# Kernel optimization log

Measured on AMD Instinct MI355X. Metric: run time of the kernel, lower is better.

Reference implementation:

```python
import jax, jax.numpy as jnp
import numpy as np

L, H, NH, NKV, HD, FF, E, K = 4, 1024, 16, 4, 64, 2048, 8, 2
B, S = 2, 2048
THETA, EPS = 10000.0, 1e-5


def setup_inputs() -> dict:
    key = jax.random.key(0)
    ks = jax.random.split(key, 12)
    sc = 0.02
    inp = {
        "hidden_states": jax.random.normal(ks[0], (B, S, H), jnp.float32),
        "ln1_w": jnp.ones((L, H), jnp.float32),
        "ln2_w": jnp.ones((L, H), jnp.float32),
        "wq": jax.random.normal(ks[1], (L, H, NH * HD), jnp.float32) * sc,
        "wk": jax.random.normal(ks[2], (L, H, NKV * HD), jnp.float32) * sc,
        "wv": jax.random.normal(ks[3], (L, H, NKV * HD), jnp.float32) * sc,
        "wo": jax.random.normal(ks[4], (L, NH * HD, H), jnp.float32) * sc,
        "wr": jax.random.normal(ks[5], (L, H, E), jnp.float32) * sc,
        "wg": jax.random.normal(ks[6], (L, E, H, FF), jnp.float32) * sc,
        "wu": jax.random.normal(ks[7], (L, E, H, FF), jnp.float32) * sc,
        "wd": jax.random.normal(ks[8], (L, E, FF, H), jnp.float32) * sc,
    }
    return inp


def _rms(x, w):
    return x * jax.lax.rsqrt(jnp.mean(x * x, axis=-1, keepdims=True) + EPS) * w


def _rope_cos_sin(seq_len, head_dim, theta):
    inv = 1.0 / (theta ** (jnp.arange(0, head_dim, 2, dtype=jnp.float32) / head_dim))
    f = jnp.arange(seq_len, dtype=jnp.float32)[:, None] * inv  # [S, HD/2]
    emb = jnp.concatenate([f, f], axis=-1)  # [S, HD]
    return jnp.cos(emb), jnp.sin(emb)


def _rot_half(x):
    h = x.shape[-1] // 2
    return jnp.concatenate([-x[..., h:], x[..., :h]], axis=-1)


def _attention(x, wq, wk, wv, wo, cos, sin, causal_bias):
    b, s, _ = x.shape
    q = (x @ wq).reshape(b, s, NH, HD).transpose(0, 2, 1, 3)   # [B,NH,S,HD]
    k = (x @ wk).reshape(b, s, NKV, HD).transpose(0, 2, 1, 3)  # [B,NKV,S,HD]
    v = (x @ wv).reshape(b, s, NKV, HD).transpose(0, 2, 1, 3)
    c = cos[None, None]
    sn = sin[None, None]
    q = q * c + _rot_half(q) * sn
    k = k * c + _rot_half(k) * sn
    rep = NH // NKV
    k = jnp.repeat(k, rep, axis=1)  # [B,NH,S,HD]
    v = jnp.repeat(v, rep, axis=1)
    scores = jnp.einsum("bhqd,bhkd->bhqk", q, k) / jnp.sqrt(jnp.asarray(HD, x.dtype))
    scores = scores + causal_bias  # [1,1,S,S] broadcast
    attn = jax.nn.softmax(scores, axis=-1)
    out = jnp.einsum("bhqk,bhkd->bhqd", attn, v)
    out = out.transpose(0, 2, 1, 3).reshape(b, s, NH * HD)
    return out @ wo


def _moe(x, wr, wg, wu, wd):
    logits = x @ wr                            # [B,S,E]
    probs = jax.nn.softmax(logits, axis=-1)
    topv, topi = jax.lax.top_k(probs, K)       # [B,S,K]
    topv = topv / jnp.sum(topv, axis=-1, keepdims=True)
    # dense per-expert combine weights [B,S,E]
    comb = jnp.sum(jax.nn.one_hot(topi, E, dtype=x.dtype) * topv[..., None], axis=-2)
    out = jnp.zeros_like(x)
    for e in range(E):  # fixed small expert count
        h = jax.nn.silu(x @ wg[e]) * (x @ wu[e])  # [B,S,FF]
        out = out + comb[..., e:e + 1] * (h @ wd[e])
    return out


def reference(hidden_states, ln1_w, ln2_w, wq, wk, wv, wo, wr, wg, wu, wd):
    s = hidden_states.shape[1]
    cos, sin = _rope_cos_sin(s, HD, THETA)
    causal_bias = jnp.where(
        jnp.tril(jnp.ones((s, s), bool))[None, None], 0.0, -1e9
    ).astype(hidden_states.dtype)
    x = hidden_states
    for l in range(L):
        res = x
        h = _rms(x, ln1_w[l])
        h = _attention(h, wq[l], wk[l], wv[l], wo[l], cos, sin, causal_bias)
        x = jnp.clip(res + h, -100.0, 100.0)
        res = x
        h = _rms(x, ln2_w[l])
        h = _moe(h, wr[l], wg[l], wu[l], wd[l])
        x = jnp.clip(res + h, -100.0, 100.0)
    return x
```

## Files before the change

kernel.cpp:

```cpp
#include <hip/hip_runtime.h>
#include <hip/hip_bf16.h>
#include <math.h>

typedef unsigned short u16;
typedef short short8 __attribute__((ext_vector_type(8)));
typedef short short4v __attribute__((ext_vector_type(4)));
typedef float f32x4 __attribute__((ext_vector_type(4)));

#define NLAYER 4
#define HDIM 1024
#define NHEAD 16
#define NKVH 4
#define FFDIM 2048
#define NEXP 8
#define SEQ 2048
#define NBATCH 2
#define NTOK (NBATCH*SEQ)
#define NPAIR (NTOK*2)
#define RMS_EPS 1e-5f

__device__ __forceinline__ u16 b16(float x) {
  union { __hip_bfloat16 h; u16 u; } c;
  c.h = __float2bfloat16(x);
  return c.u;
}
__device__ __forceinline__ float b2f(u16 b) {
  return __builtin_bit_cast(float, ((unsigned)b) << 16);
}
__device__ __forceinline__ void split2(float x, u16& o0, u16& o1) {
  o0 = b16(x); o1 = b16(x - b2f(o0));
}
__device__ __forceinline__ float clip100(float v) {
  return fminf(fmaxf(v, -100.f), 100.f);
}
__device__ __forceinline__ int swz8(int bid, int nwg) {
  return (bid & 7) * (nwg >> 3) + (bid >> 3);
}

__global__ __launch_bounds__(256)
void rmsnorm_kernel(const float* __restrict__ x, const float* __restrict__ w,
                    u16* __restrict__ oh, u16* __restrict__ ol) {
  int t = blockIdx.x, tid = threadIdx.x;
  const float* xr = x + (long)t * HDIM;
  float4 v = *(const float4*)(xr + tid * 4);
  float ss = v.x*v.x + v.y*v.y + v.z*v.z + v.w*v.w;
  #pragma unroll
  for (int m = 32; m; m >>= 1) ss += __shfl_xor(ss, m);
  __shared__ float sb[4];
  if ((tid & 63) == 0) sb[tid >> 6] = ss;
  __syncthreads();
  ss = sb[0] + sb[1] + sb[2] + sb[3];
  float sc = 1.0f / sqrtf(ss * (1.f/HDIM) + RMS_EPS);
  float4 wv = *(const float4*)(w + tid * 4);
  float ov[4] = {v.x*sc*wv.x, v.y*sc*wv.y, v.z*sc*wv.z, v.w*sc*wv.w};
  short4v hv, lv;
  #pragma unroll
  for (int j = 0; j < 4; j++) { u16 h, l; split2(ov[j], h, l); hv[j]=(short)h; lv[j]=(short)l; }
  *(short4v*)&oh[(long)t*HDIM + tid*4] = hv;
  *(short4v*)&ol[(long)t*HDIM + tid*4] = lv;
}

__global__ __launch_bounds__(256)
void rope_table_kernel(float* __restrict__ tab) {
  int idx = blockIdx.x * 256 + threadIdx.x;
  int i = idx & 31, pos = idx >> 5;
  double e = -(double)i * 0.28782313662425575;
  float inv = (float)exp(e);
  float f = (float)pos * inv;
  tab[idx] = cosf(f);
  tab[SEQ*32 + idx] = sinf(f);
}

#define GPAD 40

__device__ __forceinline__ void gemm_core128(
    const u16* __restrict__ Ah, const u16* __restrict__ Al, long arow,
    const float* __restrict__ Bp, int Nb, int bcol0, int K,
    u16 (&As)[2][128][GPAD], u16 (&Bs)[2][64][GPAD],
    int tid, int wr, int lr, int lg, f32x4 (&acc)[2][4])
{
  int a_r = tid >> 1, a_kq = (tid & 1) * 16;
  int b_col = tid & 63;
  int b_kh = (tid >> 6) * 8;
  short8 pA[4];
  float pB[8];
  short8 cBh, cBl;
  auto loadA = [&](int k0) {
    if (arow >= 0) {
      const u16* ah = Ah + arow * (long)K + k0 + a_kq;
      const u16* al = Al + arow * (long)K + k0 + a_kq;
      pA[0] = *(const short8*)ah;
      pA[1] = *(const short8*)(ah + 8);
      pA[2] = *(const short8*)al;
      pA[3] = *(const short8*)(al + 8);
    } else {
      short8 z = {0,0,0,0,0,0,0,0};
      #pragma unroll
      for (int q = 0; q < 4; q++) pA[q] = z;
    }
  };
  auto loadB = [&](int k0) {
    const float* bp = Bp + (long)(k0 + b_kh) * Nb + bcol0 + b_col;
    #pragma unroll
    for (int j = 0; j < 8; j++) pB[j] = bp[(long)j * Nb];
  };
  auto convB = [&]() {
    #pragma unroll
    for (int j = 0; j < 8; j++) {
      u16 h, l; split2(pB[j], h, l);
      cBh[j] = (short)h; cBl[j] = (short)l;
    }
  };
  loadA(0); loadB(0); convB();
  for (int k0 = 0; k0 < K; k0 += 32) {
    if (k0) __syncthreads();
    *(short8*)&As[0][a_r][a_kq]     = pA[0];
    *(short8*)&As[0][a_r][a_kq + 8] = pA[1];
    *(short8*)&As[1][a_r][a_kq]     = pA[2];
    *(short8*)&As[1][a_r][a_kq + 8] = pA[3];
    *(short8*)&Bs[0][b_col][b_kh] = cBh;
    *(short8*)&Bs[1][b_col][b_kh] = cBl;
    __syncthreads();
    int kn = k0 + 32;
    if (kn < K) { loadA(kn); loadB(kn); }
    short8 bf[2][4];
    #pragma unroll
    for (int t = 0; t < 2; t++)
      #pragma unroll
      for (int n = 0; n < 4; n++)
        bf[t][n] = *(const short8*)&Bs[t][n*16 + lr][lg*8];
    #pragma unroll
    for (int m = 0; m < 2; m++) {
      short8 afh = *(const short8*)&As[0][wr + m*16 + lr][lg*8];
      short8 afl = *(const short8*)&As[1][wr + m*16 + lr][lg*8];
      #pragma unroll
      for (int n = 0; n < 4; n++) {
        f32x4 a = acc[m][n];
        a = __builtin_amdgcn_mfma_f32_16x16x32_bf16(afh, bf[0][n], a, 0, 0, 0);
        a = __builtin_amdgcn_mfma_f32_16x16x32_bf16(afh, bf[1][n], a, 0, 0, 0);
        a = __builtin_amdgcn_mfma_f32_16x16x32_bf16(afl, bf[0][n], a, 0, 0, 0);
        acc[m][n] = a;
      }
    }
    if (kn < K) convB();
  }
}

__global__ __launch_bounds__(256)
void gemm_down(const u16* __restrict__ Ah, const u16* __restrict__ Al,
               const float* __restrict__ B, float* __restrict__ Cf,
               const int* __restrict__ offs, int N, int K, long bstride, int ncol)
{
  __shared__ u16 As[2][128][GPAD];
  __shared__ u16 Bs[2][64][GPAD];
  int nwg = gridDim.x;
  int bid = swz8(blockIdx.x, nwg);
  int cpe = nwg >> 3;
  int z = bid / cpe, rr2 = bid % cpe;
  int rs = offs[z], re = offs[z + 1];
  int brow = rr2 / ncol, bcol = rr2 % ncol;
  int p0 = rs + brow * 128;
  if (p0 >= re) return;
  int bcol0 = bcol * 64;
  const float* Bp = B + (long)z * bstride;
  int tid = threadIdx.x, wv = tid >> 6, lane = tid & 63;
  int lr = lane & 15, lg = lane >> 4;
  int wr = wv * 32;
  long arow = -1;
  { int rr = p0 + (tid >> 1); if (rr < re) arow = rr; }
  f32x4 acc[2][4];
  #pragma unroll
  for (int m = 0; m < 2; m++)
    #pragma unroll
    for (int n = 0; n < 4; n++) acc[m][n] = {0.f,0.f,0.f,0.f};
  gemm_core128(Ah, Al, arow, Bp, N, bcol0, K, As, Bs, tid, wr, lr, lg, acc);
  #pragma unroll
  for (int m = 0; m < 2; m++) {
    int row0 = p0 + wr + m*16 + lg*4;
    #pragma unroll
    for (int n = 0; n < 4; n++) {
      int col = bcol0 + n*16 + lr;
      #pragma unroll
      for (int r = 0; r < 4; r++) {
        int row = row0 + r;
        if (row < re) Cf[(long)row * N + col] = acc[m][n][r];
      }
    }
  }
}

__global__ __launch_bounds__(256)
void gemm_wo(const u16* __restrict__ Ah, const u16* __restrict__ Al,
             const float* __restrict__ B, float* __restrict__ Cf,
             int M, int N, int K, int ncol)
{
  __shared__ u16 As[2][128][GPAD];
  __shared__ u16 Bs[2][64][GPAD];
  int bid = swz8(blockIdx.x, gridDim.x);
  int brow = bid / ncol, bcol = bid % ncol;
  int p0 = brow * 128;
  int bcol0 = bcol * 64;
  int tid = threadIdx.x, wv = tid >> 6, lane = tid & 63;
  int lr = lane & 15, lg = lane >> 4;
  int wr = wv * 32;
  long arow = p0 + (tid >> 1);
  f32x4 acc[2][4];
  #pragma unroll
  for (int m = 0; m < 2; m++)
    #pragma unroll
    for (int n = 0; n < 4; n++) acc[m][n] = {0.f,0.f,0.f,0.f};
  gemm_core128(Ah, Al, arow, B, N, bcol0, K, As, Bs, tid, wr, lr, lg, acc);
  #pragma unroll
  for (int m = 0; m < 2; m++) {
    int row0 = p0 + wr + m*16 + lg*4;
    #pragma unroll
    for (int n = 0; n < 4; n++) {
      int col = bcol0 + n*16 + lr;
      #pragma unroll
      for (int r = 0; r < 4; r++) {
        long idx = (long)(row0 + r) * N + col;
        Cf[idx] = clip100(Cf[idx] + acc[m][n][r]);
      }
    }
  }
}

__global__ __launch_bounds__(256)
void gemm_gateup(const u16* __restrict__ Ah, const u16* __restrict__ Al,
                 const float* __restrict__ Bg, const float* __restrict__ Bu,
                 u16* __restrict__ Ch, u16* __restrict__ Cl,
                 const int* __restrict__ gather, const int* __restrict__ offs)
{
  __shared__ u16 As[2][128][GPAD];
  __shared__ u16 Bgs[2][64][GPAD];
  __shared__ u16 Bus[2][64][GPAD];
  const int K = HDIM, N = FFDIM;
  int nwg = gridDim.x;
  int bid = swz8(blockIdx.x, nwg);
  int cpe = nwg >> 3;
  int z = bid / cpe, rr2 = bid % cpe;
  int rs = offs[z], re = offs[z + 1];
  int brow = rr2 >> 5, bcol = rr2 & 31;
  int p0 = rs + brow * 128;
  if (p0 >= re) return;
  int bcol0 = bcol * 64;
  const float* Bpg = Bg + (long)z * ((long)HDIM * FFDIM);
  const float* Bpu = Bu + (long)z * ((long)HDIM * FFDIM);
  int tid = threadIdx.x, wv = tid >> 6, lane = tid & 63;
  int lr = lane & 15, lg = lane >> 4;
  int wr = wv * 32;
  int a_r = tid >> 1, a_kq = (tid & 1) * 16;
  long arow = -1;
  { int rr = p0 + a_r; if (rr < re) arow = gather[rr]; }
  f32x4 accg[2][4], accu[2][4];
  #pragma unroll
  for (int m = 0; m < 2; m++)
    #pragma unroll
    for (int n = 0; n < 4; n++) { accg[m][n] = {0.f,0.f,0.f,0.f}; accu[m][n] = {0.f,0.f,0.f,0.f}; }
  int b_col = tid & 63;
  int b_kh = (tid >> 6) * 8;
  short8 pA[4];
  float pBg[8], pBu[8];
  short8 cGh, cGl, cUh, cUl;
  auto loadA = [&](int k0) {
    if (arow >= 0) {
      const u16* ah = Ah + arow * (long)K + k0 + a_kq;
      const u16* al = Al + arow * (long)K + k0 + a_kq;
      pA[0] = *(const short8*)ah;
      pA[1] = *(const short8*)(ah + 8);
      pA[2] = *(const short8*)al;
      pA[3] = *(const short8*)(al + 8);
    } else {
      short8 zz = {0,0,0,0,0,0,0,0};
      #pragma unroll
      for (int q = 0; q < 4; q++) pA[q] = zz;
    }
  };
  auto loadB = [&](int k0) {
    const float* bpg = Bpg + (long)(k0 + b_kh) * N + bcol0 + b_col;
    const float* bpu = Bpu + (long)(k0 + b_kh) * N + bcol0 + b_col;
    #pragma unroll
    for (int j = 0; j < 8; j++) { pBg[j] = bpg[(long)j * N]; pBu[j] = bpu[(long)j * N]; }
  };
  auto convB = [&]() {
    #pragma unroll
    for (int j = 0; j < 8; j++) {
      u16 h, l;
      split2(pBg[j], h, l); cGh[j] = (short)h; cGl[j] = (short)l;
      split2(pBu[j], h, l); cUh[j] = (short)h; cUl[j] = (short)l;
    }
  };
  loadA(0); loadB(0); convB();
  for (int k0 = 0; k0 < K; k0 += 32) {
    if (k0) __syncthreads();
    *(short8*)&As[0][a_r][a_kq]     = pA[0];
    *(short8*)&As[0][a_r][a_kq + 8] = pA[1];
    *(short8*)&As[1][a_r][a_kq]     = pA[2];
    *(short8*)&As[1][a_r][a_kq + 8] = pA[3];
    *(short8*)&Bgs[0][b_col][b_kh] = cGh;
    *(short8*)&Bgs[1][b_col][b_kh] = cGl;
    *(short8*)&Bus[0][b_col][b_kh] = cUh;
    *(short8*)&Bus[1][b_col][b_kh] = cUl;
    __syncthreads();
    int kn = k0 + 32;
    if (kn < K) { loadA(kn); loadB(kn); }
    short8 afh[2], afl[2];
    #pragma unroll
    for (int m = 0; m < 2; m++) {
      afh[m] = *(const short8*)&As[0][wr + m*16 + lr][lg*8];
      afl[m] = *(const short8*)&As[1][wr + m*16 + lr][lg*8];
    }
    #pragma unroll
    for (int n = 0; n < 4; n++) {
      short8 bgh = *(const short8*)&Bgs[0][n*16 + lr][lg*8];
      short8 bgl = *(const short8*)&Bgs[1][n*16 + lr][lg*8];
      short8 buh = *(const short8*)&Bus[0][n*16 + lr][lg*8];
      short8 bul = *(const short8*)&Bus[1][n*16 + lr][lg*8];
      #pragma unroll
      for (int m = 0; m < 2; m++) {
        f32x4 g = accg[m][n];
        g = __builtin_amdgcn_mfma_f32_16x16x32_bf16(afh[m], bgh, g, 0, 0, 0);
        g = __builtin_amdgcn_mfma_f32_16x16x32_bf16(afh[m], bgl, g, 0, 0, 0);
        g = __builtin_amdgcn_mfma_f32_16x16x32_bf16(afl[m], bgh, g, 0, 0, 0);
        accg[m][n] = g;
        f32x4 u = accu[m][n];
        u = __builtin_amdgcn_mfma_f32_16x16x32_bf16(afh[m], buh, u, 0, 0, 0);
        u = __builtin_amdgcn_mfma_f32_16x16x32_bf16(afh[m], bul, u, 0, 0, 0);
        u = __builtin_amdgcn_mfma_f32_16x16x32_bf16(afl[m], buh, u, 0, 0, 0);
        accu[m][n] = u;
      }
    }
    if (kn < K) convB();
  }
  #pragma unroll
  for (int m = 0; m < 2; m++) {
    int row0 = p0 + wr + m*16 + lg*4;
    #pragma unroll
    for (int n = 0; n < 4; n++) {
      int col = bcol0 + n*16 + lr;
      #pragma unroll
      for (int r = 0; r < 4; r++) {
        int row = row0 + r;
        if (row < re) {
          float gv = accg[m][n][r], uv = accu[m][n][r];
          float hh = gv / (1.f + __expf(-gv)) * uv;
          u16 h, l; split2(hh, h, l);
          long idx = (long)row * N + col;
          Ch[idx] = h; Cl[idx] = l;
        }
      }
    }
  }
}

__global__ __launch_bounds__(256)
void gemm_qkv(const u16* __restrict__ Ah, const u16* __restrict__ Al,
              const float* __restrict__ wq, const float* __restrict__ wk,
              const float* __restrict__ wv_, const float* __restrict__ tab,
              u16* __restrict__ qh, u16* __restrict__ ql,
              u16* __restrict__ kh_, u16* __restrict__ kl_,
              u16* __restrict__ vth, u16* __restrict__ vtl)
{
  __shared__ u16 As[2][128][GPAD];
  __shared__ u16 Bs[2][64][GPAD];
  int bid = swz8(blockIdx.x, gridDim.x);
  int bx = bid % 24;
  int p0 = (bid / 24) * 128;
  const float* Bp; int Nb, bcol0;
  if (bx < 16)      { Bp = wq;  Nb = 1024; bcol0 = bx * 64; }
  else if (bx < 20) { Bp = wk;  Nb = 256;  bcol0 = (bx - 16) * 64; }
  else              { Bp = wv_; Nb = 256;  bcol0 = (bx - 20) * 64; }
  int K = HDIM;
  int tid = threadIdx.x, wv = tid >> 6, lane = tid & 63;
  int lr = lane & 15, lg = lane >> 4;
  int wr = wv * 32;
  long arow = p0 + (tid >> 1);
  f32x4 acc[2][4];
  #pragma unroll
  for (int m = 0; m < 2; m++)
    #pragma unroll
    for (int n = 0; n < 4; n++) acc[m][n] = {0.f,0.f,0.f,0.f};
  gemm_core128(Ah, Al, arow, Bp, Nb, bcol0, K, As, Bs, tid, wr, lr, lg, acc);
  if (bx < 16) {
    int h = bx;
    #pragma unroll
    for (int m = 0; m < 2; m++) {
      #pragma unroll
      for (int r = 0; r < 4; r++) {
        int tok = p0 + wr + m*16 + lg*4 + r;
        int pos = tok & (SEQ - 1);
        #pragma unroll
        for (int n = 0; n < 2; n++) {
          int i = n*16 + lr;
          float c = tab[pos*32 + i], s = tab[SEQ*32 + pos*32 + i];
          float x0 = acc[m][n][r], x1 = acc[m][n+2][r];
          float y0 = x0*c - x1*s, y1 = x1*c + x0*s;
          long base = (long)tok*1024 + h*64 + i;
          u16 h0, l0; split2(y0, h0, l0); qh[base] = h0; ql[base] = l0;
          u16 h1, l1; split2(y1, h1, l1); qh[base+32] = h1; ql[base+32] = l1;
        }
      }
    }
  } else if (bx < 20) {
    int kvh = bx - 16;
    #pragma unroll
    for (int m = 0; m < 2; m++) {
      #pragma unroll
      for (int r = 0; r < 4; r++) {
        int tok = p0 + wr + m*16 + lg*4 + r;
        int pos = tok & (SEQ - 1);
        #pragma unroll
        for (int n = 0; n < 2; n++) {
          int i = n*16 + lr;
          float c = tab[pos*32 + i], s = tab[SEQ*32 + pos*32 + i];
          float x0 = acc[m][n][r], x1 = acc[m][n+2][r];
          float y0 = x0*c - x1*s, y1 = x1*c + x0*s;
          long base = (long)tok*256 + kvh*64 + i;
          u16 h0, l0; split2(y0, h0, l0); kh_[base] = h0; kl_[base] = l0;
          u16 h1, l1; split2(y1, h1, l1); kh_[base+32] = h1; kl_[base+32] = l1;
        }
      }
    }
  } else {
    int kvh = bx - 20;
    #pragma unroll
    for (int m = 0; m < 2; m++) {
      #pragma unroll
      for (int r = 0; r < 4; r++) {
        int tok = p0 + wr + m*16 + lg*4 + r;
        int bb = tok >> 11, tl = tok & (SEQ - 1);
        #pragma unroll
        for (int n = 0; n < 4; n++) {
          int hd = n*16 + lr;
          u16 h0, l0; split2(acc[m][n][r], h0, l0);
          long vidx = ((long)(bb*NKVH + kvh)*64 + hd)*SEQ + tl;
          vth[vidx] = h0; vtl[vidx] = l0;
        }
      }
    }
  }
}

#define ATP 70
#define PPAD 68
__global__ __launch_bounds__(256)
void attn_kernel(const u16* __restrict__ qhi, const u16* __restrict__ qlo,
                 const u16* __restrict__ khi, const u16* __restrict__ klo,
                 const u16* __restrict__ vthi, const u16* __restrict__ vtlo,
                 u16* __restrict__ ohi, u16* __restrict__ olo)
{
  int bid = swz8(blockIdx.x, gridDim.x);
  int qp = bid & 15, h = (bid >> 4) & 15, b = bid >> 8;
  int kvh = h >> 2;
  int tid = threadIdx.x, w = tid >> 6, lane = tid & 63;
  int lr = lane & 15, lg = lane >> 4;
  __shared__ u16 KhS[64][ATP], KlS[64][ATP], VhS[64][ATP], VlS[64][ATP];
  __shared__ u16 Ps[2][4][16][PPAD];
  long tokbase = (long)b * SEQ;
  int sr = tid >> 2, scg = (tid & 3) * 16;
  const u16* vrow_h = vthi + ((long)(b*NKVH + kvh)*64 + sr)*SEQ;
  const u16* vrow_l = vtlo + ((long)(b*NKVH + kvh)*64 + sr)*SEQ;
  short8 pK[4], pV[4];
  auto loadKV = [&](int kt) {
    long kg = (tokbase + kt*64 + sr)*256 + kvh*64 + scg;
    pK[0] = *(const short8*)(khi + kg);
    pK[1] = *(const short8*)(khi + kg + 8);
    pK[2] = *(const short8*)(klo + kg);
    pK[3] = *(const short8*)(klo + kg + 8);
    long vg = kt*64 + scg;
    pV[0] = *(const short8*)(vrow_h + vg);
    pV[1] = *(const short8*)(vrow_h + vg + 8);
    pV[2] = *(const short8*)(vrow_l + vg);
    pV[3] = *(const short8*)(vrow_l + vg + 8);
  };
  loadKV(0);

  for (int ph = 0; ph < 2; ph++) {
    int qt = ph ? (31 - qp) : qp;
    long q0 = (long)qt * 64;
    const u16* qh_row = qhi + (tokbase + q0 + w*16 + lr)*1024 + h*64;
    const u16* ql_row = qlo + (tokbase + q0 + w*16 + lr)*1024 + h*64;
    short8 aqh[2], aql[2];
    #pragma unroll
    for (int hf = 0; hf < 2; hf++) {
      aqh[hf] = *(const short8*)(qh_row + hf*32 + lg*8);
      aql[hf] = *(const short8*)(ql_row + hf*32 + lg*8);
    }
    f32x4 Oacc[4];
    #pragma unroll
    for (int n = 0; n < 4; n++) Oacc[n] = {0.f,0.f,0.f,0.f};
    float mrow[4] = {-1e30f,-1e30f,-1e30f,-1e30f};
    float lrow[4] = {0.f,0.f,0.f,0.f};
    for (int kt = 0; kt <= qt; kt++) {
      if (ph | kt) __syncthreads();
      *(short8*)&KhS[sr][scg]   = pK[0];
      *(short8*)&KhS[sr][scg+8] = pK[1];
      *(short8*)&KlS[sr][scg]   = pK[2];
      *(short8*)&KlS[sr][scg+8] = pK[3];
      *(short8*)&VhS[sr][scg]   = pV[0];
      *(short8*)&VhS[sr][scg+8] = pV[1];
      *(short8*)&VlS[sr][scg]   = pV[2];
      *(short8*)&VlS[sr][scg+8] = pV[3];
      __syncthreads();
      loadKV(kt < qt ? kt + 1 : 0);
      float sv[4][4];
      #pragma unroll
      for (int n = 0; n < 4; n++) {
        short8 bh0 = *(const short8*)&KhS[n*16 + lr][lg*8];
        short8 bh1 = *(const short8*)&KhS[n*16 + lr][32 + lg*8];
        short8 bl0 = *(const short8*)&KlS[n*16 + lr][lg*8];
        short8 bl1 = *(const short8*)&KlS[n*16 + lr][32 + lg*8];
        f32x4 c = {0.f,0.f,0.f,0.f};
        c = __builtin_amdgcn_mfma_f32_16x16x32_bf16(aqh[0], bh0, c, 0, 0, 0);
        c = __builtin_amdgcn_mfma_f32_16x16x32_bf16(aqh[1], bh1, c, 0, 0, 0);
        c = __builtin_amdgcn_mfma_f32_16x16x32_bf16(aqh[0], bl0, c, 0, 0, 0);
        c = __builtin_amdgcn_mfma_f32_16x16x32_bf16(aqh[1], bl1, c, 0, 0, 0);
        c = __builtin_amdgcn_mfma_f32_16x16x32_bf16(aql[0], bh0, c, 0, 0, 0);
        c = __builtin_amdgcn_mfma_f32_16x16x32_bf16(aql[1], bh1, c, 0, 0, 0);
        #pragma unroll
        for (int r = 0; r < 4; r++) sv[n][r] = c[r] * 0.125f;
      }
      if (kt == qt) {
        #pragma unroll
        for (int n = 0; n < 4; n++)
          #pragma unroll
          for (int r = 0; r < 4; r++)
            if (n*16 + lr > w*16 + lg*4 + r) sv[n][r] = -1e30f;
      }
      float pvv[4][4], alpha[4];
      #pragma unroll
      for (int r = 0; r < 4; r++) {
        float vm = fmaxf(fmaxf(sv[0][r], sv[1][r]), fmaxf(sv[2][r], sv[3][r]));
        #pragma unroll
        for (int msk = 1; msk < 16; msk <<= 1) vm = fmaxf(vm, __shfl_xor(vm, msk));
        float mnew = fmaxf(mrow[r], vm);
        alpha[r] = __expf(mrow[r] - mnew);
        float psum = 0.f;
        #pragma unroll
        for (int n = 0; n < 4; n++) { pvv[n][r] = __expf(sv[n][r] - mnew); psum += pvv[n][r]; }
        #pragma unroll
        for (int msk = 1; msk < 16; msk <<= 1) psum += __shfl_xor(psum, msk);
        lrow[r] = lrow[r] * alpha[r] + psum;
        mrow[r] = mnew;
      }
      #pragma unroll
      for (int n = 0; n < 4; n++)
        #pragma unroll
        for (int r = 0; r < 4; r++) {
          u16 t0, t1;
          split2(pvv[n][r], t0, t1);
          Ps[0][w][lg*4 + r][n*16 + lr] = t0;
          Ps[1][w][lg*4 + r][n*16 + lr] = t1;
        }
      #pragma unroll
      for (int n = 0; n < 4; n++)
        #pragma unroll
        for (int r = 0; r < 4; r++) Oacc[n][r] *= alpha[r];
      #pragma unroll
      for (int kk = 0; kk < 2; kk++) {
        short8 aph = *(const short8*)&Ps[0][w][lr][kk*32 + lg*8];
        short8 apl = *(const short8*)&Ps[1][w][lr][kk*32 + lg*8];
        #pragma unroll
        for (int n = 0; n < 4; n++) {
          short8 bvh = *(const short8*)&VhS[n*16 + lr][kk*32 + lg*8];
          short8 bvl = *(const short8*)&VlS[n*16 + lr][kk*32 + lg*8];
          f32x4 a = Oacc[n];
          a = __builtin_amdgcn_mfma_f32_16x16x32_bf16(aph, bvh, a, 0, 0, 0);
          a = __builtin_amdgcn_mfma_f32_16x16x32_bf16(aph, bvl, a, 0, 0, 0);
          a = __builtin_amdgcn_mfma_f32_16x16x32_bf16(apl, bvh, a, 0, 0, 0);
          Oacc[n] = a;
        }
      }
    }
    u16* oh_row = ohi + (tokbase + q0 + w*16)*1024 + h*64;
    u16* ol_row = olo + (tokbase + q0 + w*16)*1024 + h*64;
    #pragma unroll
    for (int n = 0; n < 4; n++)
      #pragma unroll
      for (int r = 0; r < 4; r++) {
        float v = Oacc[n][r] / lrow[r];
        u16 h0, l0; split2(v, h0, l0);
        oh_row[(lg*4 + r)*1024 + n*16 + lr] = h0;
        ol_row[(lg*4 + r)*1024 + n*16 + lr] = l0;
      }
  }
}

__global__ __launch_bounds__(64)
void router_kernel(const float* __restrict__ x, const float* __restrict__ w2,
                   const float* __restrict__ wr, int* __restrict__ tok_e,
                   float* __restrict__ tok_w, int* __restrict__ counts)
{
  int t = blockIdx.x, l = threadIdx.x;
  const float* xr = x + (long)t * HDIM;
  float xv[16];
  float ss = 0.f;
  #pragma unroll
  for (int j = 0; j < 16; j++) { xv[j] = xr[l + j*64]; ss += xv[j]*xv[j]; }
  #pragma unroll
  for (int m = 32; m; m >>= 1) ss += __shfl_xor(ss, m);
  float sc = 1.0f / sqrtf(ss * (1.f/HDIM) + RMS_EPS);
  float acc[8] = {0,0,0,0,0,0,0,0};
  #pragma unroll
  for (int j = 0; j < 16; j++) {
    int hh = l + j*64;
    float xnv = xv[j] * sc * w2[hh];
    const float* wrow = wr + hh * 8;
    #pragma unroll
    for (int e = 0; e < 8; e++) acc[e] += xnv * wrow[e];
  }
  #pragma unroll
  for (int e = 0; e < 8; e++)
    #pragma unroll
    for (int m = 32; m; m >>= 1) acc[e] += __shfl_xor(acc[e], m);
  if (l == 0) {
    float mx = acc[0];
    #pragma unroll
    for (int e = 1; e < 8; e++) mx = fmaxf(mx, acc[e]);
    float ex[8], s = 0.f;
    #pragma unroll
    for (int e = 0; e < 8; e++) { ex[e] = expf(acc[e] - mx); s += ex[e]; }
    int e0 = 0;
    #pragma unroll
    for (int e = 1; e < 8; e++) if (ex[e] > ex[e0]) e0 = e;
    int e1 = (e0 == 0) ? 1 : 0;
    for (int e = 0; e < 8; e++) if (e != e0 && ex[e] > ex[e1]) e1 = e;
    float v0 = ex[e0] / s, v1 = ex[e1] / s, wsum = v0 + v1;
    tok_e[2*t] = e0; tok_e[2*t+1] = e1;
    tok_w[2*t] = v0 / wsum; tok_w[2*t+1] = v1 / wsum;
    atomicAdd(&counts[e0], 1);
    atomicAdd(&counts[e1], 1);
  }
}

__global__ void scan_kernel(const int* __restrict__ counts, int* __restrict__ offs,
                            int* __restrict__ cursor) {
  if (threadIdx.x == 0 && blockIdx.x == 0) {
    int s = 0;
    for (int e = 0; e < NEXP; e++) { offs[e] = s; cursor[e] = s; s += counts[e]; }
    offs[NEXP] = s;
  }
}

__global__ __launch_bounds__(256)
void scatter_kernel(const int* __restrict__ tok_e, int* __restrict__ cursor,
                    int* __restrict__ tok_of_pair, int* __restrict__ tok_slot) {
  int t = blockIdx.x * 256 + threadIdx.x;
  if (t >= NTOK) return;
  #pragma unroll
  for (int s = 0; s < 2; s++) {
    int e = tok_e[2*t + s];
    int pos = atomicAdd(&cursor[e], 1);
    tok_of_pair[pos] = t;
    tok_slot[2*t + s] = pos;
  }
}

__global__ __launch_bounds__(256)
void combine_kernel(float* __restrict__ x, const float* __restrict__ po,
                    const int* __restrict__ tok_slot, const float* __restrict__ tok_w) {
  int t = blockIdx.x, tid = threadIdx.x;
  long s0 = tok_slot[2*t], s1 = tok_slot[2*t+1];
  float w0 = tok_w[2*t], w1 = tok_w[2*t+1];
  int c = tid * 4;
  float4 xv = *(float4*)(x + (long)t*HDIM + c);
  float4 a  = *(const float4*)(po + s0*HDIM + c);
  float4 bb = *(const float4*)(po + s1*HDIM + c);
  xv.x = clip100(xv.x + w0*a.x + w1*bb.x);
  xv.y = clip100(xv.y + w0*a.y + w1*bb.y);
  xv.z = clip100(xv.z + w0*a.z + w1*bb.z);
  xv.w = clip100(xv.w + w0*a.w + w1*bb.w);
  *(float4*)(x + (long)t*HDIM + c) = xv;
}

extern "C" void kernel_launch(void* const* d_in, const int* in_sizes, int n_in,
                              void* d_out, int out_size, void* d_ws, size_t ws_size,
                              hipStream_t stream)
{
  (void)in_sizes; (void)n_in; (void)out_size; (void)ws_size;
  const float* hs  = (const float*)d_in[0];
  const float* ln1 = (const float*)d_in[1];
  const float* ln2 = (const float*)d_in[2];
  const float* wq  = (const float*)d_in[3];
  const float* wk  = (const float*)d_in[4];
  const float* wvv = (const float*)d_in[5];
  const float* wo  = (const float*)d_in[6];
  const float* wr  = (const float*)d_in[7];
  const float* wg  = (const float*)d_in[8];
  const float* wu  = (const float*)d_in[9];
  const float* wd  = (const float*)d_in[10];
  float* x = (float*)d_out;

  char* p = (char*)d_ws;
  auto carve = [&](size_t bytes) {
    char* r = p; p += (bytes + 255) & ~(size_t)255; return r;
  };
  float* tab = (float*)carve((size_t)SEQ * 32 * 2 * 4);
  u16* xnh = (u16*)carve((size_t)NTOK * HDIM * 2);
  u16* xnl = (u16*)carve((size_t)NTOK * HDIM * 2);
  char* R  = carve((size_t)128 * 1024 * 1024);
  u16* qhi = (u16*)R;
  u16* qlo = (u16*)(R + 8u*1024*1024);
  u16* khi = (u16*)(R + 16u*1024*1024);
  u16* klo = (u16*)(R + 18u*1024*1024);
  u16* vthi= (u16*)(R + 20u*1024*1024);
  u16* vtlo= (u16*)(R + 22u*1024*1024);
  u16* ohi = (u16*)(R + 24u*1024*1024);
  u16* olo = (u16*)(R + 32u*1024*1024);
  u16*   ghi = (u16*)R;
  u16*   glo = (u16*)(R + 32u*1024*1024);
  float* po  = (float*)(R + 64u*1024*1024);
  int*   tok_e       = (int*)carve(NTOK * 2 * 4);
  float* tok_w       = (float*)carve(NTOK * 2 * 4);
  int*   tok_slot    = (int*)carve(NTOK * 2 * 4);
  int*   tok_of_pair = (int*)carve(NPAIR * 4);
  int*   counts      = (int*)carve(8 * 4);
  int*   offs        = (int*)carve(9 * 4);
  int*   cursor      = (int*)carve(8 * 4);

  hipMemcpyAsync(x, hs, (size_t)NTOK * HDIM * 4, hipMemcpyDeviceToDevice, stream);
  rope_table_kernel<<<SEQ*32/256, 256, 0, stream>>>(tab);

  for (int l = 0; l < NLAYER; l++) {
    rmsnorm_kernel<<<NTOK, 256, 0, stream>>>(x, ln1 + (long)l*HDIM, xnh, xnl);
    gemm_qkv<<<768, 256, 0, stream>>>(
        xnh, xnl, wq + (long)l*HDIM*1024, wk + (long)l*HDIM*256,
        wvv + (long)l*HDIM*256, tab, qhi, qlo, khi, klo, vthi, vtlo);
    attn_kernel<<<512, 256, 0, stream>>>(
        qhi, qlo, khi, klo, vthi, vtlo, ohi, olo);
    gemm_wo<<<512, 256, 0, stream>>>(
        ohi, olo, wo + (long)l*1024*HDIM, x, NTOK, HDIM, 1024, 16);

    rmsnorm_kernel<<<NTOK, 256, 0, stream>>>(x, ln2 + (long)l*HDIM, xnh, xnl);
    hipMemsetAsync(counts, 0, 8 * 4, stream);
    router_kernel<<<NTOK, 64, 0, stream>>>(
        x, ln2 + (long)l*HDIM, wr + (long)l*HDIM*NEXP, tok_e, tok_w, counts);
    scan_kernel<<<1, 64, 0, stream>>>(counts, offs, cursor);
    scatter_kernel<<<NTOK/256, 256, 0, stream>>>(tok_e, cursor, tok_of_pair, tok_slot);
    gemm_gateup<<<16384, 256, 0, stream>>>(
        xnh, xnl, wg + (long)l*NEXP*HDIM*FFDIM, wu + (long)l*NEXP*HDIM*FFDIM,
        ghi, glo, tok_of_pair, offs);
    gemm_down<<<8192, 256, 0, stream>>>(
        ghi, glo, wd + (long)l*NEXP*FFDIM*HDIM, po,
        offs, HDIM, FFDIM, (long)FFDIM*HDIM, 16);
    combine_kernel<<<NTOK, 256, 0, stream>>>(x, po, tok_slot, tok_w);
  }
}
```

Baseline: 3.305 ms.

## Group MoE GEMM tiles for cache reuse and use 2x2 wave layout in gateup

Block indices in gemm_gateup and gemm_down are remapped so that consecutive workgroups of each expert cover 4x8 groups of row and column tiles rather than sweeping a full row of columns, which should improve L2 reuse of both activations and weights. gemm_gateup also changes the per-wave tiling from 32x64 to 64x32 (2x2 waves), so each wave loads fewer B fragments from LDS for every A fragment. The grouped mapping assumes the per-expert row-tile count is a multiple of the group size, and the early-exit check still skips empty tiles.

```diff
diff --git a/kernel.cpp b/kernel.cpp
--- a/kernel.cpp
+++ b/kernel.cpp
@@ -149,16 +149,18 @@
 __global__ __launch_bounds__(256)
 void gemm_down(const u16* __restrict__ Ah, const u16* __restrict__ Al,
                const float* __restrict__ B, float* __restrict__ Cf,
-               const int* __restrict__ offs, int N, int K, long bstride, int ncol)
+               const int* __restrict__ offs, int N, int K, long bstride)
 {
   __shared__ u16 As[2][128][GPAD];
   __shared__ u16 Bs[2][64][GPAD];
   int nwg = gridDim.x;
   int bid = swz8(blockIdx.x, nwg);
   int cpe = nwg >> 3;
-  int z = bid / cpe, rr2 = bid % cpe;
+  int z = bid / cpe, u = bid % cpe;
+  int g = u >> 5, w2 = u & 31;
+  int brow = (g >> 1) * 4 + (w2 >> 3);
+  int bcol = (g & 1) * 8 + (w2 & 7);
   int rs = offs[z], re = offs[z + 1];
-  int brow = rr2 / ncol, bcol = rr2 % ncol;
   int p0 = rs + brow * 128;
   if (p0 >= re) return;
   int bcol0 = bcol * 64;
@@ -238,9 +240,11 @@
   int nwg = gridDim.x;
   int bid = swz8(blockIdx.x, nwg);
   int cpe = nwg >> 3;
-  int z = bid / cpe, rr2 = bid % cpe;
+  int z = bid / cpe, u = bid % cpe;
+  int g = u >> 5, w2 = u & 31;
+  int brow = (g >> 2) * 4 + (w2 >> 3);
+  int bcol = (g & 3) * 8 + (w2 & 7);
   int rs = offs[z], re = offs[z + 1];
-  int brow = rr2 >> 5, bcol = rr2 & 31;
   int p0 = rs + brow * 128;
   if (p0 >= re) return;
   int bcol0 = bcol * 64;
@@ -248,15 +252,15 @@
   const float* Bpu = Bu + (long)z * ((long)HDIM * FFDIM);
   int tid = threadIdx.x, wv = tid >> 6, lane = tid & 63;
   int lr = lane & 15, lg = lane >> 4;
-  int wr = wv * 32;
+  int wrow = (wv >> 1) * 64, wcol = (wv & 1) * 32;
   int a_r = tid >> 1, a_kq = (tid & 1) * 16;
   long arow = -1;
   { int rr = p0 + a_r; if (rr < re) arow = gather[rr]; }
-  f32x4 accg[2][4], accu[2][4];
-  #pragma unroll
-  for (int m = 0; m < 2; m++)
-    #pragma unroll
-    for (int n = 0; n < 4; n++) { accg[m][n] = {0.f,0.f,0.f,0.f}; accu[m][n] = {0.f,0.f,0.f,0.f}; }
+  f32x4 accg[4][2], accu[4][2];
+  #pragma unroll
+  for (int m = 0; m < 4; m++)
+    #pragma unroll
+    for (int n = 0; n < 2; n++) { accg[m][n] = {0.f,0.f,0.f,0.f}; accu[m][n] = {0.f,0.f,0.f,0.f}; }
   int b_col = tid & 63;
   int b_kh = (tid >> 6) * 8;
   short8 pA[4];
@@ -304,40 +308,40 @@
     __syncthreads();
     int kn = k0 + 32;
     if (kn < K) { loadA(kn); loadB(kn); }
-    short8 afh[2], afl[2];
-    #pragma unroll
-    for (int m = 0; m < 2; m++) {
-      afh[m] = *(const short8*)&As[0][wr + m*16 + lr][lg*8];
-      afl[m] = *(const short8*)&As[1][wr + m*16 + lr][lg*8];
-    }
-    #pragma unroll
-    for (int n = 0; n < 4; n++) {
-      short8 bgh = *(const short8*)&Bgs[0][n*16 + lr][lg*8];
-      short8 bgl = *(const short8*)&Bgs[1][n*16 + lr][lg*8];
-      short8 buh = *(const short8*)&Bus[0][n*16 + lr][lg*8];
-      short8 bul = *(const short8*)&Bus[1][n*16 + lr][lg*8];
-      #pragma unroll
-      for (int m = 0; m < 2; m++) {
-        f32x4 g = accg[m][n];
-        g = __builtin_amdgcn_mfma_f32_16x16x32_bf16(afh[m], bgh, g, 0, 0, 0);
-        g = __builtin_amdgcn_mfma_f32_16x16x32_bf16(afh[m], bgl, g, 0, 0, 0);
-        g = __builtin_amdgcn_mfma_f32_16x16x32_bf16(afl[m], bgh, g, 0, 0, 0);
-        accg[m][n] = g;
-        f32x4 u = accu[m][n];
-        u = __builtin_amdgcn_mfma_f32_16x16x32_bf16(afh[m], buh, u, 0, 0, 0);
-        u = __builtin_amdgcn_mfma_f32_16x16x32_bf16(afh[m], bul, u, 0, 0, 0);
-        u = __builtin_amdgcn_mfma_f32_16x16x32_bf16(afl[m], buh, u, 0, 0, 0);
-        accu[m][n] = u;
+    short8 afh[4], afl[4];
+    #pragma unroll
+    for (int m = 0; m < 4; m++) {
+      afh[m] = *(const short8*)&As[0][wrow + m*16 + lr][lg*8];
+      afl[m] = *(const short8*)&As[1][wrow + m*16 + lr][lg*8];
+    }
+    #pragma unroll
+    for (int n = 0; n < 2; n++) {
+      short8 bgh = *(const short8*)&Bgs[0][wcol + n*16 + lr][lg*8];
+      short8 bgl = *(const short8*)&Bgs[1][wcol + n*16 + lr][lg*8];
+      short8 buh = *(const short8*)&Bus[0][wcol + n*16 + lr][lg*8];
+      short8 bul = *(const short8*)&Bus[1][wcol + n*16 + lr][lg*8];
+      #pragma unroll
+      for (int m = 0; m < 4; m++) {
+        f32x4 g2 = accg[m][n];
+        g2 = __builtin_amdgcn_mfma_f32_16x16x32_bf16(afh[m], bgh, g2, 0, 0, 0);
+        g2 = __builtin_amdgcn_mfma_f32_16x16x32_bf16(afh[m], bgl, g2, 0, 0, 0);
+        g2 = __builtin_amdgcn_mfma_f32_16x16x32_bf16(afl[m], bgh, g2, 0, 0, 0);
+        accg[m][n] = g2;
+        f32x4 u2 = accu[m][n];
+        u2 = __builtin_amdgcn_mfma_f32_16x16x32_bf16(afh[m], buh, u2, 0, 0, 0);
+        u2 = __builtin_amdgcn_mfma_f32_16x16x32_bf16(afh[m], bul, u2, 0, 0, 0);
+        u2 = __builtin_amdgcn_mfma_f32_16x16x32_bf16(afl[m], buh, u2, 0, 0, 0);
+        accu[m][n] = u2;
       }
     }
     if (kn < K) convB();
   }
   #pragma unroll
-  for (int m = 0; m < 2; m++) {
-    int row0 = p0 + wr + m*16 + lg*4;
-    #pragma unroll
-    for (int n = 0; n < 4; n++) {
-      int col = bcol0 + n*16 + lr;
+  for (int m = 0; m < 4; m++) {
+    int row0 = p0 + wrow + m*16 + lg*4;
+    #pragma unroll
+    for (int n = 0; n < 2; n++) {
+      int col = bcol0 + wcol + n*16 + lr;
       #pragma unroll
       for (int r = 0; r < 4; r++) {
         int row = row0 + r;
@@ -742,7 +746,7 @@
         ghi, glo, tok_of_pair, offs);
     gemm_down<<<8192, 256, 0, stream>>>(
         ghi, glo, wd + (long)l*NEXP*FFDIM*HDIM, po,
-        offs, HDIM, FFDIM, (long)FFDIM*HDIM, 16);
+        offs, HDIM, FFDIM, (long)FFDIM*HDIM);
     combine_kernel<<<NTOK, 256, 0, stream>>>(x, po, tok_slot, tok_w);
   }
 }
```

Result: slower. 3.521 ms (+6.5%).
